# Optimization experiments

Hardware: AMD Instinct MI355X
Metric: run time of the kernel (lower is better)

## Reference

```python
import jax, jax.numpy as jnp
import numpy as np

HIDDEN_DIM = 256
TOP_K = 16
TEMPERATURE = 1.0
SCALE = 1.0 / np.sqrt(HIDDEN_DIM)


def setup_inputs() -> dict:
    key = jax.random.key(0)
    k1, k2, k3, k4 = jax.random.split(key, 4)
    B, N, D = 32, 32768, 256
    # xavier-uniform-ish scale for square projections
    lim = np.sqrt(6.0 / (D + HIDDEN_DIM))
    return {
        "query": jax.random.normal(k1, (B, D), dtype=jnp.float32),
        "keys": jax.random.normal(k2, (B, N, D), dtype=jnp.float32),
        "Wq": jax.random.uniform(k3, (HIDDEN_DIM, D), dtype=jnp.float32, minval=-lim, maxval=lim),
        "Wk": jax.random.uniform(k4, (HIDDEN_DIM, D), dtype=jnp.float32, minval=-lim, maxval=lim),
        "segment_offset": 16384,
    }


def reference(query, keys, Wq, Wk, segment_offset):
    # query: [B, D]; keys: [B, N, D]; Wq/Wk: [H, D] (torch Linear layout)
    pq = query @ Wq.T                      # [B, H]
    pk = jnp.einsum("bnd,hd->bnh", keys, Wk)  # [B, N, H]
    scores = jnp.einsum("bh,bnh->bn", pq, pk) * SCALE  # [B, N]
    num_keys = keys.shape[1]
    # causal mask: positions >= segment_offset are masked out
    if 0 < segment_offset < num_keys:
        mask = jnp.arange(num_keys) >= segment_offset  # [N]
        scores = jnp.where(mask[None, :], -jnp.inf, scores)
    top_scores, top_indices = jax.lax.top_k(scores, TOP_K)  # [B, K]
    routing_weights = jax.nn.softmax(top_scores / TEMPERATURE, axis=-1)
    return routing_weights, top_indices, scores
```

## Files before the change

### kernel.cpp

```cpp
#include <hip/hip_runtime.h>
#include <math.h>

#define B 32
#define N 32768
#define D 256
#define H 256
#define TOPK 16
#define SCALE (1.0f / 16.0f)
#define TEMPERATURE 1.0f
#define MASK_FILL (-3.0e38f)

__global__ __launch_bounds__(256) void proj_kernel(const float* __restrict__ q,
                                                   const float* __restrict__ Wq,
                                                   const float* __restrict__ Wk,
                                                   float* __restrict__ v) {
    int b = blockIdx.x;
    int t = threadIdx.x;
    __shared__ float qs[D];
    __shared__ float pq[H];
    qs[t] = q[b * D + t];
    __syncthreads();
    float acc = 0.f;
    const float* wrow = Wq + t * D;
    #pragma unroll 4
    for (int d = 0; d < D; d += 4) {
        acc += wrow[d] * qs[d] + wrow[d + 1] * qs[d + 1] +
               wrow[d + 2] * qs[d + 2] + wrow[d + 3] * qs[d + 3];
    }
    pq[t] = acc;
    __syncthreads();
    float vv = 0.f;
    #pragma unroll 4
    for (int h = 0; h < H; ++h) vv += Wk[h * D + t] * pq[h];
    v[b * D + t] = vv * SCALE;
}

__global__ __launch_bounds__(256) void score_kernel(const float* __restrict__ keys,
                                                    const float* __restrict__ v,
                                                    const int* __restrict__ segp,
                                                    float* __restrict__ scores) {
    int seg = *segp;
    int limit = (seg > 0 && seg < N) ? seg : N;
    int lane = threadIdx.x & 63;
    int wave = threadIdx.x >> 6;
    long long row0 = (long long)blockIdx.x * 256 + (long long)wave * 64;
    int b = (int)(row0 / N);
    int n0 = (int)(row0 % N);

    if (n0 + 64 <= limit) {
        float4 v4 = *(const float4*)(v + b * D + lane * 4);
        const float* kb = keys + ((long long)b * N + n0) * D + lane * 4;
        for (int r = 0; r < 64; ++r) {
            float4 k4 = *(const float4*)(kb + (long long)r * D);
            float p = k4.x * v4.x + k4.y * v4.y + k4.z * v4.z + k4.w * v4.w;
            #pragma unroll
            for (int m = 32; m >= 1; m >>= 1) p += __shfl_xor(p, m, 64);
            if (lane == 0) scores[(long long)b * N + n0 + r] = p;
        }
    } else if (n0 >= limit) {
        scores[(long long)b * N + n0 + lane] = MASK_FILL;
    } else {
        float4 v4 = *(const float4*)(v + b * D + lane * 4);
        const float* kb = keys + ((long long)b * N) * D;
        for (int r = 0; r < 64; ++r) {
            int n = n0 + r;
            float s;
            if (n < limit) {
                float4 k4 = *(const float4*)(kb + (long long)n * D + lane * 4);
                float p = k4.x * v4.x + k4.y * v4.y + k4.z * v4.z + k4.w * v4.w;
                #pragma unroll
                for (int m = 32; m >= 1; m >>= 1) p += __shfl_xor(p, m, 64);
                s = p;
            } else {
                s = MASK_FILL;
            }
            if (lane == 0) scores[(long long)b * N + n] = s;
        }
    }
}

#define MAXE (N / 256)
__global__ __launch_bounds__(256, 1) void topk_kernel(const float* __restrict__ scores,
                                                      const int* __restrict__ segp,
                                                      float* __restrict__ out_w,
                                                      float* __restrict__ out_i) {
    int b = blockIdx.x;
    int t = threadIdx.x;
    int seg = *segp;
    int limit = (seg > 0 && seg < N) ? seg : N;

    float val[MAXE];
    #pragma unroll
    for (int k = 0; k < MAXE; ++k) {
        int idx = k * 256 + t;
        val[k] = (idx < limit) ? scores[(long long)b * N + idx] : -INFINITY;
    }

    __shared__ float swin_s[TOPK];
    __shared__ int   swin_i[TOPK];
    __shared__ float red_s[4];
    __shared__ int   red_i[4];

    float last_s = INFINITY;
    int   last_i = -1;

    for (int r = 0; r < TOPK; ++r) {
        float bs = -INFINITY;
        int   bi = 0x7fffffff;
        #pragma unroll
        for (int k = 0; k < MAXE; ++k) {
            int idx = k * 256 + t;
            float s = val[k];
            bool after_last = (s < last_s) || (s == last_s && idx > last_i);
            bool beats      = (s > bs)     || (s == bs && idx < bi);
            if (after_last && beats) { bs = s; bi = idx; }
        }
        #pragma unroll
        for (int m = 1; m < 64; m <<= 1) {
            float os = __shfl_xor(bs, m, 64);
            int   oi = __shfl_xor(bi, m, 64);
            if ((os > bs) || (os == bs && oi < bi)) { bs = os; bi = oi; }
        }
        int wv = t >> 6;
        if ((t & 63) == 0) { red_s[wv] = bs; red_i[wv] = bi; }
        __syncthreads();
        if (t == 0) {
            for (int w = 1; w < 4; ++w) {
                if ((red_s[w] > bs) || (red_s[w] == bs && red_i[w] < bi)) {
                    bs = red_s[w]; bi = red_i[w];
                }
            }
            swin_s[r] = bs; swin_i[r] = bi;
        }
        __syncthreads();
        last_s = swin_s[r];
        last_i = swin_i[r];
    }

    if (t < 64) {
        float e = 0.f;
        float m = swin_s[0];
        if (t < TOPK) e = expf((swin_s[t] - m) / TEMPERATURE);
        float sum = e;
        #pragma unroll
        for (int mo = 1; mo < 64; mo <<= 1) sum += __shfl_xor(sum, mo, 64);
        if (t < TOPK) {
            out_w[b * TOPK + t] = e / sum;
            out_i[b * TOPK + t] = (float)swin_i[t];
        }
    }
}

extern "C" void kernel_launch(void* const* d_in, const int* in_sizes, int n_in,
                              void* d_out, int out_size, void* d_ws, size_t ws_size,
                              hipStream_t stream) {
    const float* q    = (const float*)d_in[0];
    const float* keys = (const float*)d_in[1];
    const float* Wq   = (const float*)d_in[2];
    const float* Wk   = (const float*)d_in[3];
    const int*   seg  = (const int*)d_in[4];

    float* out    = (float*)d_out;
    float* out_w  = out;
    float* out_i  = out + B * TOPK;
    float* scores = out + 2 * B * TOPK;

    float* v = (float*)d_ws;

    proj_kernel<<<B, 256, 0, stream>>>(q, Wq, Wk, v);
    score_kernel<<<(B * N) / 256, 256, 0, stream>>>(keys, v, seg, scores);
    topk_kernel<<<B, 256, 0, stream>>>(scores, seg, out_w, out_i);
}
```

Measured before the change: 1.404 ms.

## Replace per-row shuffle reductions with LDS transpose reduction in score kernel

The score kernel now issues all 64 row loads per wave into registers up front, then writes the 64 partial dot products to a swizzled LDS tile and reads them back transposed, so each lane sums one row and stores it with a coalesced write. This replaces 64 serial six-step shuffle reductions and single-lane stores per wave. Block size is halved to 128 threads to fit 32 KB of LDS per block. The trade-offs are higher register pressure from the 64-entry partial array and LDS occupancy limits, but the kernel is memory-bound on the keys tensor, so more loads in flight may matter more.

```diff
diff --git a/kernel.cpp b/kernel.cpp
--- a/kernel.cpp
+++ b/kernel.cpp
@@ -35,7 +35,7 @@
     v[b * D + t] = vv * SCALE;
 }
 
-__global__ __launch_bounds__(256) void score_kernel(const float* __restrict__ keys,
+__global__ __launch_bounds__(128) void score_kernel(const float* __restrict__ keys,
                                                     const float* __restrict__ v,
                                                     const int* __restrict__ segp,
                                                     float* __restrict__ scores) {
@@ -43,25 +43,47 @@
     int limit = (seg > 0 && seg < N) ? seg : N;
     int lane = threadIdx.x & 63;
     int wave = threadIdx.x >> 6;
-    long long row0 = (long long)blockIdx.x * 256 + (long long)wave * 64;
-    int b = (int)(row0 / N);
-    int n0 = (int)(row0 % N);
+    __shared__ float T[2][64][64];
+    float* Tw = &T[wave][0][0];
+
+    int row0 = blockIdx.x * 128 + wave * 64;
+    int b  = row0 >> 15;
+    int n0 = row0 & (N - 1);
+    long long rowbase = (long long)b * N + n0;
 
     if (n0 + 64 <= limit) {
         float4 v4 = *(const float4*)(v + b * D + lane * 4);
-        const float* kb = keys + ((long long)b * N + n0) * D + lane * 4;
+        const float* kb = keys + rowbase * D + lane * 4;
+
+        float p[64];
+        #pragma unroll
         for (int r = 0; r < 64; ++r) {
-            float4 k4 = *(const float4*)(kb + (long long)r * D);
-            float p = k4.x * v4.x + k4.y * v4.y + k4.z * v4.z + k4.w * v4.w;
-            #pragma unroll
-            for (int m = 32; m >= 1; m >>= 1) p += __shfl_xor(p, m, 64);
-            if (lane == 0) scores[(long long)b * N + n0 + r] = p;
+            float4 k4 = *(const float4*)(kb + (size_t)r * D);
+            p[r] = k4.x * v4.x + k4.y * v4.y + k4.z * v4.z + k4.w * v4.w;
         }
+
+        int l4  = lane & 3;
+        int lhi = lane >> 2;
+        int lx  = lane & 15;
+        #pragma unroll
+        for (int r = 0; r < 64; ++r) {
+            Tw[r * 64 + (l4 | (((lhi ^ (r & 15)) & 15) << 2))] = p[r];
+        }
+        asm volatile("s_waitcnt lgkmcnt(0)" ::: "memory");
+        __builtin_amdgcn_sched_barrier(0);
+
+        float ax = 0.f, ay = 0.f, az = 0.f, aw = 0.f;
+        #pragma unroll
+        for (int j = 0; j < 16; ++j) {
+            const float4 qv = *(const float4*)(Tw + lane * 64 + ((j ^ lx) << 2));
+            ax += qv.x; ay += qv.y; az += qv.z; aw += qv.w;
+        }
+        scores[rowbase + lane] = (ax + ay) + (az + aw);
     } else if (n0 >= limit) {
-        scores[(long long)b * N + n0 + lane] = MASK_FILL;
+        scores[rowbase + lane] = MASK_FILL;
     } else {
         float4 v4 = *(const float4*)(v + b * D + lane * 4);
-        const float* kb = keys + ((long long)b * N) * D;
+        const float* kb = keys + (long long)b * N * D;
         for (int r = 0; r < 64; ++r) {
             int n = n0 + r;
             float s;
@@ -168,6 +190,6 @@
     float* v = (float*)d_ws;
 
     proj_kernel<<<B, 256, 0, stream>>>(q, Wq, Wk, v);
-    score_kernel<<<(B * N) / 256, 256, 0, stream>>>(keys, v, seg, scores);
+    score_kernel<<<(B * N) / 128, 128, 0, stream>>>(keys, v, seg, scores);
     topk_kernel<<<B, 256, 0, stream>>>(scores, seg, out_w, out_i);
 }
```

After: 1.401 ms. No clear change (-0.2%).
